# Optimization experiments

Measured on AMD Instinct MI355X. Metric: run time of the kernel, lower is better.

The kernel has to match this reference:

```python
import jax, jax.numpy as jnp
import numpy as np

NUM_HEADS = 16


def setup_inputs() -> dict:
    key = jax.random.key(0)
    ks = jax.random.split(key, 9)
    B, N, E = 2, 2048, 1024
    s = 1.0 / np.sqrt(E).astype(np.float32)
    inp = {"x": jax.random.normal(ks[0], (B, N, E), jnp.float32)}
    names = ["q", "k", "v", "o"]
    for i, n in enumerate(names):
        inp[f"W{n}"] = jax.random.normal(ks[1 + 2 * i], (E, E), jnp.float32) * s
        inp[f"b{n}"] = jax.random.normal(ks[2 + 2 * i], (E,), jnp.float32) * 0.01
    return inp


def _feature(x):
    # act_fun = '1+elu'
    return jax.nn.elu(x) + 1.0


def reference(x, Wq, bq, Wk, bk, Wv, bv, Wo, bo):
    B, N, E = x.shape
    H = NUM_HEADS
    d = E // H

    def proj(t, W, b):  # torch nn.Linear: t @ W^T + b
        return t @ W.T + b

    def split_heads(t):  # (B,N,E) -> (B,H,N,d)
        return t.reshape(B, N, H, d).transpose(0, 2, 1, 3)

    q = _feature(split_heads(proj(x, Wq, bq)))
    k = _feature(split_heads(proj(x, Wk, bk)))
    v = split_heads(proj(x, Wv, bv))

    # causal linear attention: o_t = q_t @ cumsum_{s<=t} (k_s v_s^T)
    kv = jnp.cumsum(k[..., :, None] * v[..., None, :], axis=2)  # (B,H,N,d,d)
    o = jnp.einsum('bhnd,bhnde->bhne', q, kv)                   # (B,H,N,d)

    o = o.transpose(0, 2, 1, 3).reshape(B, N, E)
    return o @ Wo.T + bo
```

## Files before the change

### kernel.cpp

```cpp
#include <hip/hip_runtime.h>
#include <hip/hip_bf16.h>
#include <cmath>

typedef unsigned short u16;
typedef __bf16 bf16x8 __attribute__((ext_vector_type(8)));
typedef float  f32x4  __attribute__((ext_vector_type(4)));
typedef float  f4     __attribute__((ext_vector_type(4)));
typedef u16    us4    __attribute__((ext_vector_type(4)));

#define DEVFN __device__ __forceinline__

static constexpr int Bq = 2, Nq = 2048, Eq = 1024;
static constexpr int Mq = Bq * Nq;
static constexpr int CHK = 64;
static constexpr int NC  = Nq / CHK;
static constexpr int BH  = Bq * 16;

DEVFN u16 f2b(float f) {
    union { float f; unsigned int u; } x; x.f = f;
    unsigned int r = x.u + 0x7fffu + ((x.u >> 16) & 1u);
    return (u16)(r >> 16);
}
DEVFN float b2f(u16 v) {
    union { unsigned int u; float f; } x; x.u = ((unsigned int)v) << 16; return x.f;
}

DEVFN void gl_lds16(const u16* g, u16* l) {
    __builtin_amdgcn_global_load_lds(
        (const __attribute__((address_space(1))) unsigned int*)(g),
        (__attribute__((address_space(3))) unsigned int*)(l),
        16, 0, 0);
}

__global__ __launch_bounds__(256)
void cvt_all_kernel(const float* __restrict__ x,
                    const float* __restrict__ w0, const float* __restrict__ w1,
                    const float* __restrict__ w2, const float* __restrict__ w3,
                    u16* __restrict__ Xb, u16* __restrict__ Wb)
{
    const int blk = blockIdx.x;
    const float* s; u16* d; int i;
    if (blk < 4096) {
        i = blk * 256 + threadIdx.x;  s = x;  d = Xb;
    } else {
        const int wsel = (blk - 4096) >> 10;
        i = ((blk - 4096) & 1023) * 256 + threadIdx.x;
        s = (wsel == 0) ? w0 : (wsel == 1) ? w1 : (wsel == 2) ? w2 : w3;
        d = Wb + (size_t)wsel * (Eq * Eq);
    }
    f4 v = *reinterpret_cast<const f4*>(&s[(size_t)i * 4]);
    us4 p; p[0] = f2b(v[0]); p[1] = f2b(v[1]); p[2] = f2b(v[2]); p[3] = f2b(v[3]);
    *reinterpret_cast<us4*>(&d[(size_t)i * 4]) = p;
}

__global__ __launch_bounds__(512, 2)
void qkv8_kernel(const u16* __restrict__ X, const u16* __restrict__ W,
                 const float* __restrict__ b0, const float* __restrict__ b1,
                 const float* __restrict__ b2,
                 u16* __restrict__ Qb, u16* __restrict__ Kb, u16* __restrict__ KbT,
                 u16* __restrict__ VbT)
{
    __shared__ u16 lds[3 * 16384];
    const int tid = threadIdx.x, wid = tid >> 6, lane = tid & 63;
    const int wm = wid >> 2, wn = wid & 3;
    const int fr = lane & 15, fq = lane >> 4;

    const int bid = blockIdx.x;
    const int fid = (bid & 7) * 24 + (bid >> 3);
    const int bx = fid % 12, by = fid / 12;
    const int m0 = by * 256, n0 = bx * 256;

    const int ra = tid >> 2;
    const int sc = ((tid & 3) ^ ((tid >> 3) & 3)) * 8;
    const u16* gA = X + (size_t)(m0 + ra) * 1024 + sc;
    const u16* gB = W + (size_t)(n0 + ra) * 1024 + sc;
    const int dw = wid * 512;

    const int fsw = (fq ^ ((fr >> 1) & 3)) << 3;
    int aoff[2][4], boff[4];
#pragma unroll
    for (int h = 0; h < 2; ++h)
#pragma unroll
        for (int j = 0; j < 4; ++j)
            aoff[h][j] = (wm * 128 + h * 64 + j * 16 + fr) * 32 + fsw;
#pragma unroll
    for (int j = 0; j < 4; ++j)
        boff[j] = 8192 + (wn * 64 + j * 16 + fr) * 32 + fsw;

#define STA(kt, bs) do { u16* _b = lds + (bs) * 16384 + dw;                      \
        gl_lds16(gA + (kt) * 32,              _b);                               \
        gl_lds16(gA + (kt) * 32 + 128 * 1024, _b + 4096); } while (0)
#define STB(kt, bs) do { u16* _b = lds + (bs) * 16384 + 8192 + dw;               \
        gl_lds16(gB + (kt) * 32,              _b);                               \
        gl_lds16(gB + (kt) * 32 + 128 * 1024, _b + 4096); } while (0)

    STA(0, 0); STB(0, 0);
    STA(1, 1); STB(1, 1);
    asm volatile("s_waitcnt vmcnt(4)" ::: "memory");
    __builtin_amdgcn_sched_barrier(0);
    __builtin_amdgcn_s_barrier();

    f32x4 acc[8][4] = {};
    int cb = 0, sb = 2;

    for (int t = 0; t < 32; ++t) {
        const u16* buf = lds + cb * 16384;
        bf16x8 a[4], b[4];
#pragma unroll
        for (int j = 0; j < 4; ++j)
            a[j] = *reinterpret_cast<const bf16x8*>(&buf[aoff[0][j]]);
#pragma unroll
        for (int j = 0; j < 4; ++j)
            b[j] = *reinterpret_cast<const bf16x8*>(&buf[boff[j]]);
        if (t + 2 < 32) STA(t + 2, sb);
        __builtin_amdgcn_s_barrier();
        __builtin_amdgcn_s_setprio(1);
#pragma unroll
        for (int j = 0; j < 4; ++j)
#pragma unroll
            for (int n = 0; n < 4; ++n)
                acc[j][n] = __builtin_amdgcn_mfma_f32_16x16x32_bf16(
                    a[j], b[n], acc[j][n], 0, 0, 0);
        __builtin_amdgcn_s_setprio(0);
        __builtin_amdgcn_s_barrier();
#pragma unroll
        for (int j = 0; j < 4; ++j)
            a[j] = *reinterpret_cast<const bf16x8*>(&buf[aoff[1][j]]);
        if (t + 2 < 32) STB(t + 2, sb);
        __builtin_amdgcn_s_barrier();
        __builtin_amdgcn_s_setprio(1);
#pragma unroll
        for (int j = 0; j < 4; ++j)
#pragma unroll
            for (int n = 0; n < 4; ++n)
                acc[4 + j][n] = __builtin_amdgcn_mfma_f32_16x16x32_bf16(
                    a[j], b[n], acc[4 + j][n], 0, 0, 0);
        __builtin_amdgcn_s_setprio(0);
        if (t < 30)       asm volatile("s_waitcnt vmcnt(4)" ::: "memory");
        else if (t == 30) asm volatile("s_waitcnt vmcnt(0)" ::: "memory");
        __builtin_amdgcn_sched_barrier(0);
        __builtin_amdgcn_s_barrier();
        cb = (cb == 2) ? 0 : cb + 1;
        sb = (sb == 2) ? 0 : sb + 1;
    }
#undef STA
#undef STB

    const int nw  = n0 + wn * 64;
    const int seg = nw >> 10;
    const float* bp = (seg == 0) ? b0 : (seg == 1) ? b1 : b2;
#pragma unroll
    for (int mg = 0; mg < 8; ++mg)
#pragma unroll
        for (int ni = 0; ni < 4; ++ni) {
            const int nl    = ((nw & 1023) + ni * 16 + fr);
            const int mbase = m0 + wm * 128 + mg * 16 + fq * 4;
            const float bn  = bp[nl];
            float vr[4];
#pragma unroll
            for (int r = 0; r < 4; ++r) {
                float v = acc[mg][ni][r] + bn;
                if (seg < 2) v = (v > 0.f) ? (v + 1.f) : __expf(v);
                vr[r] = v;
            }
            if (seg == 0) {
#pragma unroll
                for (int r = 0; r < 4; ++r)
                    Qb[(size_t)(mbase + r) * 1024 + nl] = f2b(vr[r]);
            } else {
                us4 pk;
#pragma unroll
                for (int r = 0; r < 4; ++r) pk[r] = f2b(vr[r]);
                const int bb = mbase >> 11, nt = mbase & 2047;
                const int hh = nl >> 6,     dd = nl & 63;
                u16* T = (seg == 1) ? KbT : VbT;
                *reinterpret_cast<us4*>(
                    &T[((size_t)(bb * 16 + hh) * 64 + dd) * 2048 + nt]) = pk;
                if (seg == 1) {
#pragma unroll
                    for (int r = 0; r < 4; ++r)
                        Kb[(size_t)(mbase + r) * 1024 + nl] = f2b(vr[r]);
                }
            }
        }
}

__global__ __launch_bounds__(256)
void oproj_kernel(const u16* __restrict__ X, const u16* __restrict__ W,
                  const float* __restrict__ b0, float* __restrict__ outF)
{
    constexpr int BUFU = (64 + 128) * 32;
    __shared__ u16 lds[3 * BUFU];
    const int tid = threadIdx.x, wid = tid >> 6, lane = tid & 63;
    const int wr = (wid >> 1) * 32, wc = (wid & 1) * 64;
    const int fr = lane & 15, fq = lane >> 4;

    const int bid = blockIdx.x;
    const int fid = (bid & 7) * 64 + (bid >> 3);
    const int bx = fid & 7, by = fid >> 3;
    const int m0 = by * 64, n0 = bx * 128;

    const int ra = tid >> 2;
    const int sc = ((tid & 3) ^ ((tid >> 3) & 3)) * 8;
    const u16* gA = X + (size_t)(m0 + ra) * 1024 + sc;
    const u16* gB = W + (size_t)(n0 + ra) * 1024 + sc;
    const int dw = wid * 512;

    const int fsw = (fq ^ ((fr >> 1) & 3)) << 3;
    int aoff[2], boff[4];
#pragma unroll
    for (int mi = 0; mi < 2; ++mi) aoff[mi] = (wr + mi * 16 + fr) * 32 + fsw;
#pragma unroll
    for (int ni = 0; ni < 4; ++ni) boff[ni] = 2048 + (wc + ni * 16 + fr) * 32 + fsw;

#define STAGE(kt, bs) do { u16* _b = lds + (bs) * BUFU;                          \
        gl_lds16(gA + (kt) * 32,             _b + dw);                           \
        gl_lds16(gB + (kt) * 32,             _b + 2048 + dw);                    \
        gl_lds16(gB + (kt) * 32 + 64 * 1024, _b + 4096 + dw); } while (0)

    STAGE(0, 0);
    STAGE(1, 1);
    asm volatile("s_waitcnt vmcnt(3)" ::: "memory");
    __builtin_amdgcn_sched_barrier(0);
    __builtin_amdgcn_s_barrier();

    f32x4 acc[2][4] = {};
    int cb = 0, sb = 2;

    for (int t = 0; t < 32; ++t) {
        if (t + 2 < 32) STAGE(t + 2, sb);
        const u16* buf = lds + cb * BUFU;
        bf16x8 af[2], bfv[4];
#pragma unroll
        for (int mi = 0; mi < 2; ++mi)
            af[mi] = *reinterpret_cast<const bf16x8*>(&buf[aoff[mi]]);
#pragma unroll
        for (int ni = 0; ni < 4; ++ni)
            bfv[ni] = *reinterpret_cast<const bf16x8*>(&buf[boff[ni]]);
        __builtin_amdgcn_s_setprio(1);
#pragma unroll
        for (int mi = 0; mi < 2; ++mi)
#pragma unroll
            for (int ni = 0; ni < 4; ++ni)
                acc[mi][ni] = __builtin_amdgcn_mfma_f32_16x16x32_bf16(
                    af[mi], bfv[ni], acc[mi][ni], 0, 0, 0);
        __builtin_amdgcn_s_setprio(0);
        if (t < 30)       asm volatile("s_waitcnt vmcnt(3)" ::: "memory");
        else if (t == 30) asm volatile("s_waitcnt vmcnt(0)" ::: "memory");
        __builtin_amdgcn_sched_barrier(0);
        __builtin_amdgcn_s_barrier();
        cb = (cb == 2) ? 0 : cb + 1;
        sb = (sb == 2) ? 0 : sb + 1;
    }
#undef STAGE

#pragma unroll
    for (int mi = 0; mi < 2; ++mi)
#pragma unroll
        for (int ni = 0; ni < 4; ++ni) {
            const int n     = n0 + wc + ni * 16 + fr;
            const int mbase = m0 + wr + mi * 16 + fq * 4;
            const float bn  = b0[n];
#pragma unroll
            for (int r = 0; r < 4; ++r)
                outF[(size_t)(mbase + r) * 1024 + n] = acc[mi][ni][r] + bn;
        }
}

__global__ __launch_bounds__(64)
void chunk_kv_kernel(const u16* __restrict__ KbT, const u16* __restrict__ VbT,
                     u16* __restrict__ KVT)
{
    const int blk = blockIdx.x;
    const int bh = blk >> 5, c = blk & 31;
    const int lane = threadIdx.x;
    const int fr = lane & 15, fq = lane >> 4, fk = fq * 8;
    const u16* kt = KbT + (size_t)bh * 64 * 2048;
    const u16* vt = VbT + (size_t)bh * 64 * 2048;

    bf16x8 a[4][2], b[4][2];
#pragma unroll
    for (int mi = 0; mi < 4; ++mi)
#pragma unroll
        for (int kh = 0; kh < 2; ++kh)
            a[mi][kh] = *reinterpret_cast<const bf16x8*>(
                &vt[(size_t)(mi * 16 + fr) * 2048 + c * 64 + kh * 32 + fk]);
#pragma unroll
    for (int ni = 0; ni < 4; ++ni)
#pragma unroll
        for (int kh = 0; kh < 2; ++kh)
            b[ni][kh] = *reinterpret_cast<const bf16x8*>(
                &kt[(size_t)(ni * 16 + fr) * 2048 + c * 64 + kh * 32 + fk]);

    f32x4 acc[4][4] = {};
    __builtin_amdgcn_s_setprio(1);
#pragma unroll
    for (int mi = 0; mi < 4; ++mi)
#pragma unroll
        for (int ni = 0; ni < 4; ++ni)
#pragma unroll
            for (int kh = 0; kh < 2; ++kh)
                acc[mi][ni] = __builtin_amdgcn_mfma_f32_16x16x32_bf16(
                    a[mi][kh], b[ni][kh], acc[mi][ni], 0, 0, 0);
    __builtin_amdgcn_s_setprio(0);

    u16* out = KVT + (size_t)blk * 4096;
#pragma unroll
    for (int mi = 0; mi < 4; ++mi)
#pragma unroll
        for (int ni = 0; ni < 4; ++ni)
#pragma unroll
            for (int r = 0; r < 4; ++r)
                out[(mi * 16 + fq * 4 + r) * 64 + ni * 16 + fr] = f2b(acc[mi][ni][r]);
}

__global__ __launch_bounds__(256)
void scan_kernel(const u16* __restrict__ KVT, u16* __restrict__ STb)
{
    const int bh = blockIdx.x >> 4, sl = blockIdx.x & 15;
    const int el = sl * 256 + threadIdx.x;
    const u16* src = KVT + (size_t)bh * NC * 4096 + el;
    u16*      dst  = STb + (size_t)bh * NC * 4096 + el;
    float run = 0.f;
#pragma unroll 4
    for (int c = 0; c < NC; ++c) {
        dst[(size_t)c * 4096] = f2b(run);
        run += b2f(src[(size_t)c * 4096]);
    }
}

__global__ __launch_bounds__(64)
void attn_kernel(const u16* __restrict__ Qb, const u16* __restrict__ Kb,
                 const u16* __restrict__ VbT, const u16* __restrict__ STb,
                 u16* __restrict__ Ob)
{
    __shared__ u16 P[64 * 72];
    const int blk = blockIdx.x;
    const int bh = blk >> 5, c = blk & 31;
    const int b = bh >> 4, h = bh & 15;
    const int lane = threadIdx.x;
    const int fr = lane & 15, fq = lane >> 4, fk = fq * 8;
    const int tok0 = b * 2048 + c * 64;

    bf16x8 qa[4][2];
#pragma unroll
    for (int mi = 0; mi < 4; ++mi)
#pragma unroll
        for (int kh = 0; kh < 2; ++kh)
            qa[mi][kh] = *reinterpret_cast<const bf16x8*>(
                &Qb[(size_t)(tok0 + mi * 16 + fr) * 1024 + h * 64 + kh * 32 + fk]);

    {
        bf16x8 kb[4][2];
#pragma unroll
        for (int si = 0; si < 4; ++si)
#pragma unroll
            for (int kh = 0; kh < 2; ++kh)
                kb[si][kh] = *reinterpret_cast<const bf16x8*>(
                    &Kb[(size_t)(tok0 + si * 16 + fr) * 1024 + h * 64 + kh * 32 + fk]);
        f32x4 p[4][4] = {};
        __builtin_amdgcn_s_setprio(1);
#pragma unroll
        for (int mi = 0; mi < 4; ++mi)
#pragma unroll
            for (int si = 0; si < 4; ++si)
#pragma unroll
                for (int kh = 0; kh < 2; ++kh)
                    p[mi][si] = __builtin_amdgcn_mfma_f32_16x16x32_bf16(
                        qa[mi][kh], kb[si][kh], p[mi][si], 0, 0, 0);
        __builtin_amdgcn_s_setprio(0);
#pragma unroll
        for (int mi = 0; mi < 4; ++mi)
#pragma unroll
            for (int si = 0; si < 4; ++si)
#pragma unroll
                for (int r = 0; r < 4; ++r) {
                    int t = mi * 16 + fq * 4 + r;
                    int s = si * 16 + fr;
                    float v = (s <= t) ? p[mi][si][r] : 0.0f;
                    P[t * 72 + s] = f2b(v);
                }
    }
    __syncthreads();

    f32x4 acc[4][4] = {};
    {
        const u16* st = STb + (size_t)blk * 4096;
        bf16x8 sb[4][2];
#pragma unroll
        for (int ni = 0; ni < 4; ++ni)
#pragma unroll
            for (int kh = 0; kh < 2; ++kh)
                sb[ni][kh] = *reinterpret_cast<const bf16x8*>(
                    &st[(ni * 16 + fr) * 64 + kh * 32 + fk]);
        __builtin_amdgcn_s_setprio(1);
#pragma unroll
        for (int mi = 0; mi < 4; ++mi)
#pragma unroll
            for (int ni = 0; ni < 4; ++ni)
#pragma unroll
                for (int kh = 0; kh < 2; ++kh)
                    acc[mi][ni] = __builtin_amdgcn_mfma_f32_16x16x32_bf16(
                        qa[mi][kh], sb[ni][kh], acc[mi][ni], 0, 0, 0);
        __builtin_amdgcn_s_setprio(0);
    }
    {
        const u16* vt = VbT + (size_t)bh * 64 * 2048;
#pragma unroll
        for (int sh = 0; sh < 2; ++sh) {
            bf16x8 pa[4], vb[4];
#pragma unroll
            for (int mi = 0; mi < 4; ++mi)
                pa[mi] = *reinterpret_cast<const bf16x8*>(
                    &P[(mi * 16 + fr) * 72 + sh * 32 + fk]);
#pragma unroll
            for (int ni = 0; ni < 4; ++ni)
                vb[ni] = *reinterpret_cast<const bf16x8*>(
                    &vt[(size_t)(ni * 16 + fr) * 2048 + c * 64 + sh * 32 + fk]);
            __builtin_amdgcn_s_setprio(1);
#pragma unroll
            for (int mi = 0; mi < 4; ++mi)
#pragma unroll
                for (int ni = 0; ni < 4; ++ni)
                    acc[mi][ni] = __builtin_amdgcn_mfma_f32_16x16x32_bf16(
                        pa[mi], vb[ni], acc[mi][ni], 0, 0, 0);
            __builtin_amdgcn_s_setprio(0);
        }
    }
#pragma unroll
    for (int mi = 0; mi < 4; ++mi)
#pragma unroll
        for (int ni = 0; ni < 4; ++ni)
#pragma unroll
            for (int r = 0; r < 4; ++r) {
                int t = tok0 + mi * 16 + fq * 4 + r;
                int n = h * 64 + ni * 16 + fr;
                Ob[(size_t)t * 1024 + n] = f2b(acc[mi][ni][r]);
            }
}

extern "C" void kernel_launch(void* const* d_in, const int* in_sizes, int n_in,
                              void* d_out, int out_size, void* d_ws, size_t ws_size,
                              hipStream_t stream)
{
    (void)in_sizes; (void)n_in; (void)out_size; (void)ws_size;
    const float* x  = (const float*)d_in[0];
    const float* Wq = (const float*)d_in[1];
    const float* bq = (const float*)d_in[2];
    const float* Wk = (const float*)d_in[3];
    const float* bk = (const float*)d_in[4];
    const float* Wv = (const float*)d_in[5];
    const float* bv = (const float*)d_in[6];
    const float* Wo = (const float*)d_in[7];
    const float* bo = (const float*)d_in[8];
    float* out = (float*)d_out;

    char* ws = (char*)d_ws;
    constexpr size_t SZ_ME = (size_t)Mq * Eq * 2;
    u16*   Qb  = (u16*)  (ws + 0 * SZ_ME);
    u16*   Kb  = (u16*)  (ws + 1 * SZ_ME);
    u16*   KbT = (u16*)  (ws + 2 * SZ_ME);
    u16*   VbT = (u16*)  (ws + 3 * SZ_ME);
    u16*   Ob  = (u16*)  (ws + 4 * SZ_ME);
    u16*   KVT = (u16*)  (ws + 5 * SZ_ME);
    u16*   STb = (u16*)  (ws + 6 * SZ_ME);
    u16*   Xb  = (u16*)  (ws + 7 * SZ_ME);
    u16*   Wb0 = (u16*)  (ws + 8 * SZ_ME);
    u16* Wqkvb = Wb0;
    u16* Wob   = Wb0 + (size_t)3 * Eq * Eq;

    cvt_all_kernel<<<dim3(8192), dim3(256), 0, stream>>>(x, Wq, Wk, Wv, Wo, Xb, Wb0);

    qkv8_kernel<<<dim3(192), dim3(512), 0, stream>>>(
        Xb, Wqkvb, bq, bk, bv, Qb, Kb, KbT, VbT);

    chunk_kv_kernel<<<dim3(BH * NC), dim3(64), 0, stream>>>(KbT, VbT, KVT);
    scan_kernel<<<dim3(BH * 16), dim3(256), 0, stream>>>(KVT, STb);
    attn_kernel<<<dim3(BH * NC), dim3(64), 0, stream>>>(Qb, Kb, VbT, STb, Ob);

    oproj_kernel<<<dim3(512), dim3(256), 0, stream>>>(Ob, Wob, bo, out);
}
```

Before: 95.36 us.

## Replace 256x256 QKV GEMM tile with 128x128 ring-buffered tile kernel

The fused QKV projection GEMM moves from 256x256 tiles with 512 threads to 128x128 tiles with 256 threads and 768 blocks. The K-loop now issues one combined A/B stage per iteration with a single LDS read phase instead of the split two-half schedule. This raises the block count so the GPU's compute units get more work and wave occupancy improves. In exchange, each tile reuses less data, so there is more global and LDS traffic per FLOP and fewer MFMAs sit between barriers.

```diff
diff --git a/kernel.cpp b/kernel.cpp
--- a/kernel.cpp
+++ b/kernel.cpp
@@ -53,88 +53,69 @@
     *reinterpret_cast<us4*>(&d[(size_t)i * 4]) = p;
 }
 
-__global__ __launch_bounds__(512, 2)
-void qkv8_kernel(const u16* __restrict__ X, const u16* __restrict__ W,
-                 const float* __restrict__ b0, const float* __restrict__ b1,
-                 const float* __restrict__ b2,
-                 u16* __restrict__ Qb, u16* __restrict__ Kb, u16* __restrict__ KbT,
-                 u16* __restrict__ VbT)
-{
-    __shared__ u16 lds[3 * 16384];
+__global__ __launch_bounds__(256)
+void qkv_ring(const u16* __restrict__ X, const u16* __restrict__ W,
+              const float* __restrict__ b0, const float* __restrict__ b1,
+              const float* __restrict__ b2,
+              u16* __restrict__ Qb, u16* __restrict__ Kb, u16* __restrict__ KbT,
+              u16* __restrict__ VbT)
+{
+    constexpr int BUFU = 8192;
+    __shared__ u16 lds[3 * BUFU];
     const int tid = threadIdx.x, wid = tid >> 6, lane = tid & 63;
-    const int wm = wid >> 2, wn = wid & 3;
+    const int wr = (wid >> 1) * 64, wc = (wid & 1) * 64;
     const int fr = lane & 15, fq = lane >> 4;
 
     const int bid = blockIdx.x;
-    const int fid = (bid & 7) * 24 + (bid >> 3);
-    const int bx = fid % 12, by = fid / 12;
-    const int m0 = by * 256, n0 = bx * 256;
-
-    const int ra = tid >> 2;
-    const int sc = ((tid & 3) ^ ((tid >> 3) & 3)) * 8;
-    const u16* gA = X + (size_t)(m0 + ra) * 1024 + sc;
-    const u16* gB = W + (size_t)(n0 + ra) * 1024 + sc;
+    const int fid = (bid & 7) * 96 + (bid >> 3);
+    const int bx = fid % 24, by = fid / 24;
+    const int m0 = by * 128, n0 = bx * 128;
+
+    const int row0 = tid >> 2;
+    const int sc   = ((tid & 3) ^ ((row0 >> 1) & 3)) * 8;
+    const u16* gA = X + (size_t)(m0 + row0) * 1024 + sc;
+    const u16* gB = W + (size_t)(n0 + row0) * 1024 + sc;
     const int dw = wid * 512;
 
     const int fsw = (fq ^ ((fr >> 1) & 3)) << 3;
-    int aoff[2][4], boff[4];
-#pragma unroll
-    for (int h = 0; h < 2; ++h)
-#pragma unroll
-        for (int j = 0; j < 4; ++j)
-            aoff[h][j] = (wm * 128 + h * 64 + j * 16 + fr) * 32 + fsw;
-#pragma unroll
-    for (int j = 0; j < 4; ++j)
-        boff[j] = 8192 + (wn * 64 + j * 16 + fr) * 32 + fsw;
-
-#define STA(kt, bs) do { u16* _b = lds + (bs) * 16384 + dw;                      \
-        gl_lds16(gA + (kt) * 32,              _b);                               \
-        gl_lds16(gA + (kt) * 32 + 128 * 1024, _b + 4096); } while (0)
-#define STB(kt, bs) do { u16* _b = lds + (bs) * 16384 + 8192 + dw;               \
-        gl_lds16(gB + (kt) * 32,              _b);                               \
-        gl_lds16(gB + (kt) * 32 + 128 * 1024, _b + 4096); } while (0)
-
-    STA(0, 0); STB(0, 0);
-    STA(1, 1); STB(1, 1);
+    int aoff[4], boff[4];
+#pragma unroll
+    for (int mi = 0; mi < 4; ++mi) aoff[mi] = (wr + mi * 16 + fr) * 32 + fsw;
+#pragma unroll
+    for (int ni = 0; ni < 4; ++ni) boff[ni] = 4096 + (wc + ni * 16 + fr) * 32 + fsw;
+
+#define STAGE(kt, bs) do { u16* _b = lds + (bs) * BUFU;                        \
+        gl_lds16(gA + (kt) * 32,             _b + dw);                         \
+        gl_lds16(gA + (kt) * 32 + 64 * 1024, _b + 2048 + dw);                  \
+        gl_lds16(gB + (kt) * 32,             _b + 4096 + dw);                  \
+        gl_lds16(gB + (kt) * 32 + 64 * 1024, _b + 6144 + dw); } while (0)
+
+    STAGE(0, 0);
+    STAGE(1, 1);
     asm volatile("s_waitcnt vmcnt(4)" ::: "memory");
     __builtin_amdgcn_sched_barrier(0);
     __builtin_amdgcn_s_barrier();
 
-    f32x4 acc[8][4] = {};
+    f32x4 acc[4][4] = {};
     int cb = 0, sb = 2;
 
     for (int t = 0; t < 32; ++t) {
-        const u16* buf = lds + cb * 16384;
-        bf16x8 a[4], b[4];
-#pragma unroll
-        for (int j = 0; j < 4; ++j)
-            a[j] = *reinterpret_cast<const bf16x8*>(&buf[aoff[0][j]]);
-#pragma unroll
-        for (int j = 0; j < 4; ++j)
-            b[j] = *reinterpret_cast<const bf16x8*>(&buf[boff[j]]);
-        if (t + 2 < 32) STA(t + 2, sb);
-        __builtin_amdgcn_s_barrier();
+        if (t + 2 < 32) STAGE(t + 2, sb);
+        const u16* buf = lds + cb * BUFU;
+        bf16x8 af[4], bfv[4];
+#pragma unroll
+        for (int mi = 0; mi < 4; ++mi)
+            af[mi] = *reinterpret_cast<const bf16x8*>(&buf[aoff[mi]]);
+#pragma unroll
+        for (int ni = 0; ni < 4; ++ni)
+            bfv[ni] = *reinterpret_cast<const bf16x8*>(&buf[boff[ni]]);
         __builtin_amdgcn_s_setprio(1);
 #pragma unroll
-        for (int j = 0; j < 4; ++j)
-#pragma unroll
-            for (int n = 0; n < 4; ++n)
-                acc[j][n] = __builtin_amdgcn_mfma_f32_16x16x32_bf16(
-                    a[j], b[n], acc[j][n], 0, 0, 0);
-        __builtin_amdgcn_s_setprio(0);
-        __builtin_amdgcn_s_barrier();
-#pragma unroll
-        for (int j = 0; j < 4; ++j)
-            a[j] = *reinterpret_cast<const bf16x8*>(&buf[aoff[1][j]]);
-        if (t + 2 < 32) STB(t + 2, sb);
-        __builtin_amdgcn_s_barrier();
-        __builtin_amdgcn_s_setprio(1);
-#pragma unroll
-        for (int j = 0; j < 4; ++j)
-#pragma unroll
-            for (int n = 0; n < 4; ++n)
-                acc[4 + j][n] = __builtin_amdgcn_mfma_f32_16x16x32_bf16(
-                    a[j], b[n], acc[4 + j][n], 0, 0, 0);
+        for (int mi = 0; mi < 4; ++mi)
+#pragma unroll
+            for (int ni = 0; ni < 4; ++ni)
+                acc[mi][ni] = __builtin_amdgcn_mfma_f32_16x16x32_bf16(
+                    af[mi], bfv[ni], acc[mi][ni], 0, 0, 0);
         __builtin_amdgcn_s_setprio(0);
         if (t < 30)       asm volatile("s_waitcnt vmcnt(4)" ::: "memory");
         else if (t == 30) asm volatile("s_waitcnt vmcnt(0)" ::: "memory");
@@ -143,23 +124,21 @@
         cb = (cb == 2) ? 0 : cb + 1;
         sb = (sb == 2) ? 0 : sb + 1;
     }
-#undef STA
-#undef STB
-
-    const int nw  = n0 + wn * 64;
-    const int seg = nw >> 10;
+#undef STAGE
+
+    const int seg = n0 >> 10;
     const float* bp = (seg == 0) ? b0 : (seg == 1) ? b1 : b2;
 #pragma unroll
-    for (int mg = 0; mg < 8; ++mg)
+    for (int mi = 0; mi < 4; ++mi)
 #pragma unroll
         for (int ni = 0; ni < 4; ++ni) {
-            const int nl    = ((nw & 1023) + ni * 16 + fr);
-            const int mbase = m0 + wm * 128 + mg * 16 + fq * 4;
+            const int nl    = (n0 & 1023) + wc + ni * 16 + fr;
+            const int mbase = m0 + wr + mi * 16 + fq * 4;
             const float bn  = bp[nl];
             float vr[4];
 #pragma unroll
             for (int r = 0; r < 4; ++r) {
-                float v = acc[mg][ni][r] + bn;
+                float v = acc[mi][ni][r] + bn;
                 if (seg < 2) v = (v > 0.f) ? (v + 1.f) : __expf(v);
                 vr[r] = v;
             }
@@ -471,7 +450,7 @@
 
     cvt_all_kernel<<<dim3(8192), dim3(256), 0, stream>>>(x, Wq, Wk, Wv, Wo, Xb, Wb0);
 
-    qkv8_kernel<<<dim3(192), dim3(512), 0, stream>>>(
+    qkv_ring<<<dim3(768), dim3(256), 0, stream>>>(
         Xb, Wqkvb, bq, bk, bv, Qb, Kb, KbT, VbT);
 
     chunk_kv_kernel<<<dim3(BH * NC), dim3(64), 0, stream>>>(KbT, VbT, KVT);
```

Measured after the change: 92.06 us. 3.5% less time.
